# Kernel tuning notes

Hardware: AMD Instinct MI355X
Metric: run time of the kernel (lower is better)

Reference implementation:

```python
import jax, jax.numpy as jnp
import numpy as np
from jax import lax

DIM = 256
PROJ = 128
NPOS = 8          # ceil(log2(2*64+5))
EXT = 64          # attnExtension
NLAYERS = 4
HEADS = 4
KDIM = PROJ + NPOS
EPS = 1e-5


def _ln(x):
    # LayerNorm over last dim, no affine (elementwise_affine=False)
    mu = jnp.mean(x, axis=-1, keepdims=True)
    var = jnp.mean(jnp.square(x - mu), axis=-1, keepdims=True)
    return (x - mu) * lax.rsqrt(var + EPS)


def setup_inputs() -> dict:
    key = jax.random.key(0)
    ks = jax.random.split(key, 18)
    L = 2048
    s = 0.05
    return {
        "input": jax.random.normal(ks[0], (L, PROJ), jnp.float32),
        "residual": jax.random.normal(ks[1], (5 * L, DIM), jnp.float32),
        "W_proj": jax.random.normal(ks[2], (5 * DIM, KDIM), jnp.float32) * s,
        "b_proj": jnp.zeros((5 * DIM,), jnp.float32),
        "Wq": jax.random.normal(ks[3], (DIM, DIM), jnp.float32) * s,
        "bq": jnp.zeros((DIM,), jnp.float32),
        "Wk": jax.random.normal(ks[4], (DIM, KDIM), jnp.float32) * s,
        "bk": jnp.zeros((DIM,), jnp.float32),
        "Wv": jax.random.normal(ks[5], (DIM, KDIM), jnp.float32) * s,
        "bv": jnp.zeros((DIM,), jnp.float32),
        "Wo": jax.random.normal(ks[6], (DIM, DIM), jnp.float32) * s,
        "bo": jnp.zeros((DIM,), jnp.float32),
        "conv_w": jax.random.normal(ks[7], (NLAYERS, DIM, DIM, 3), jnp.float32) * s,
        "conv_b": jnp.zeros((NLAYERS, DIM), jnp.float32),
        "W_skip": jax.random.normal(ks[8], (DIM, DIM), jnp.float32) * s,
        "b_skip": jnp.zeros((DIM,), jnp.float32),
    }


def reference(input, residual, W_proj, b_proj, Wq, bq, Wk, bk, Wv, bv,
              Wo, bo, conv_w, conv_b, W_skip, b_skip):
    L = input.shape[0]
    T = 5 * L  # tgt length
    hd = DIM // HEADS

    # positional embeddings: pos[:, i] = (arange(L) % 2^(i+1)) / 2^i
    n = jnp.arange(L, dtype=input.dtype)[:, None]
    i = jnp.arange(NPOS, dtype=input.dtype)[None, :]
    pos = jnp.mod(n, 2.0 ** (i + 1.0)) / (2.0 ** i)

    src = jnp.concatenate([input, pos], axis=1)            # (L, KDIM)
    tgt = (src @ W_proj.T + b_proj).reshape(T, DIM)        # (5L, DIM)

    # banded mask: row j may attend col i iff 5i-EXT <= j < 5i+5+EXT
    j = jnp.arange(T)[:, None]
    ii = jnp.arange(L)[None, :]
    d = j - 5 * ii
    allowed = (d >= -EXT) & (d < 5 + EXT)                  # (5L, L)

    # multihead attention (eval mode, dropout skipped)
    q = (tgt @ Wq.T + bq).reshape(T, HEADS, hd).transpose(1, 0, 2)
    k = (src @ Wk.T + bk).reshape(L, HEADS, hd).transpose(1, 0, 2)
    v = (src @ Wv.T + bv).reshape(L, HEADS, hd).transpose(1, 0, 2)
    scores = jnp.einsum('hqd,hkd->hqk', q, k) / jnp.sqrt(jnp.asarray(hd, q.dtype))
    scores = jnp.where(allowed[None], scores, -jnp.inf)
    attn = jax.nn.softmax(scores, axis=-1)
    ctx = jnp.einsum('hqk,hkd->hqd', attn, v).transpose(1, 0, 2).reshape(T, DIM)
    attn_out = ctx @ Wo.T + bo

    cnn_in = _ln(attn_out) + residual                      # (5L, DIM)

    # spectral-norm conv stack (weights assumed pre-normalized) + tanh
    x = cnn_in.T[None]                                     # (1, DIM, 5L)
    for l in range(NLAYERS):
        x = jnp.tanh(
            lax.conv_general_dilated(x, conv_w[l], window_strides=(1,),
                                     padding=[(1, 1)])
            + conv_b[l][None, :, None])
    cnn_out = x[0].T                                       # (5L, DIM)

    return _ln(cnn_out + cnn_in @ W_skip.T + b_skip)
```

## Files before the change

### kernel.cpp

```cpp
#include <hip/hip_runtime.h>
#include <hip/hip_bf16.h>

#define PROJ 128
#define KPAD 192
#define EPS 1e-5f

typedef __attribute__((ext_vector_type(4))) float f32x4;
typedef __attribute__((ext_vector_type(8))) short bf16x8;
typedef __attribute__((ext_vector_type(4))) unsigned int u32x4;

__device__ inline float bflo(unsigned u){ union{unsigned x;float f;}c; c.x = u<<16; return c.f; }
__device__ inline float bfhi(unsigned u){ union{unsigned x;float f;}c; c.x = u & 0xffff0000u; return c.f; }
__device__ inline float bf2f(unsigned short u){ union{unsigned x;float f;}c; c.x = ((unsigned)u)<<16; return c.f; }
__device__ inline unsigned short f2bf(float f){
    union{float f; unsigned u;} c; c.f = f;
    unsigned r = c.u + 0x7fff + ((c.u >> 16) & 1);
    return (unsigned short)(r >> 16);
}
__device__ __forceinline__ bf16x8 asbf(u32x4 u){ union{u32x4 a; bf16x8 b;} c; c.a = u; return c.b; }

__global__ __launch_bounds__(256) void prep_all(
    const float* __restrict__ W_proj, const float* __restrict__ Wq,
    const float* __restrict__ Wk, const float* __restrict__ Wv,
    const float* __restrict__ Wo, const float* __restrict__ Ws,
    const float* __restrict__ convw, const float* __restrict__ input,
    const float* __restrict__ bq, const float* __restrict__ b_proj,
    unsigned short* __restrict__ Wqb, unsigned short* __restrict__ Wkb,
    unsigned short* __restrict__ Wvb, unsigned short* __restrict__ Wob,
    unsigned short* __restrict__ Wsb, unsigned short* __restrict__ Wcb,
    unsigned short* __restrict__ WpbT, unsigned short* __restrict__ srcb,
    unsigned short* __restrict__ cinp, float* __restrict__ zbias,
    float* __restrict__ bqc, int L, int T)
{
    int idx = blockIdx.x * 256 + threadIdx.x;
    if (idx < 81920) {
        int w = idx >> 6, lanei = idx & 63;
        int r = w >> 8, o = w & 255;
        const float* wrow = Wq + (size_t)o * 256;
        const float* bp = b_proj + r * 256;
        float s = 0.f;
        #pragma unroll
        for (int c = 0; c < 256; c += 64) s += wrow[c + lanei] * bp[c + lanei];
        #pragma unroll
        for (int m = 32; m > 0; m >>= 1) s += __shfl_xor(s, m, 64);
        if (lanei == 0) bqc[w] = s + bq[o];
        return;
    }
    idx -= 81920;
    if (idx < 65536) { Wqb[idx] = f2bf(Wq[idx]); return; }
    idx -= 65536;
    if (idx < 49152) {
        int r = idx / 192, c = idx % 192;
        Wkb[idx] = (c < 136) ? f2bf(Wk[(size_t)r * 136 + c]) : (unsigned short)0;
        return;
    }
    idx -= 49152;
    if (idx < 49152) {
        int r = idx / 192, c = idx % 192;
        Wvb[idx] = (c < 136) ? f2bf(Wv[(size_t)r * 136 + c]) : (unsigned short)0;
        return;
    }
    idx -= 49152;
    if (idx < 65536) { Wob[idx] = f2bf(Wo[idx]); return; }
    idx -= 65536;
    if (idx < 65536) {
        int e = idx & 7;
        int lane = (idx >> 3) & 63;
        int fr = (idx >> 9) & 3;
        int wid = (idx >> 11) & 7;
        int kt = idx >> 14;
        int j = fr >> 1, ks = fr & 1;
        int kq = lane >> 4, rowf = lane & 15;
        int o = wid * 32 + j * 16 + rowf;
        int c = kt * 64 + ks * 32 + kq * 8 + e;
        Wsb[idx] = f2bf(Ws[(size_t)o * 256 + c]);
        return;
    }
    idx -= 65536;
    if (idx < 786432) {
        int e = idx & 7;
        int lane = (idx >> 3) & 63;
        int fr = (idx >> 9) & 3;
        int wid = (idx >> 11) & 7;
        int ktl = idx >> 14;
        int l = ktl / 12, kt = ktl % 12;
        int j = fr >> 1, ks = fr & 1;
        int kq = lane >> 4, rowf = lane & 15;
        int o = wid * 32 + j * 16 + rowf;
        int c = kt * 64 + ks * 32 + kq * 8 + e;
        int ktap = c >> 8, ci = c & 255;
        Wcb[idx] = f2bf(convw[(((size_t)l * 256 + o) * 256 + ci) * 3 + ktap]);
        return;
    }
    idx -= 786432;
    if (idx < 327680) {
        int r = idx >> 16;
        int rem = idx & 65535;
        int c = rem >> 8, d = rem & 255;
        WpbT[idx] = (c < 136) ? f2bf(W_proj[(size_t)(r * 256 + d) * 136 + c])
                              : (unsigned short)0;
        return;
    }
    idx -= 327680;
    if (idx < L * KPAD) {
        int n = idx / KPAD, c = idx % KPAD;
        float v = 0.f;
        if (c < PROJ) v = input[(size_t)n * PROJ + c];
        else if (c < PROJ + 8) {
            int i = c - PROJ;
            int mask = (2 << i) - 1;
            v = (float)(n & mask) / (float)(1 << i);
        }
        srcb[idx] = f2bf(v);
        return;
    }
    idx -= L * KPAD;
    if (idx < 512) {
        int row = idx >> 8, c = idx & 255;
        size_t o = (row == 0) ? (size_t)c : (size_t)(T + 1) * 256 + c;
        cinp[o] = 0;
        return;
    }
    idx -= 512;
    if (idx < 256) { zbias[idx] = 0.f; return; }
}

__device__ __forceinline__ void gemm_core_64x128(
    unsigned short (&As)[64][72], unsigned short (&Bs)[128][72],
    const unsigned short* __restrict__ A, int lda,
    const unsigned short* __restrict__ B, int ldb,
    const float* __restrict__ bias,
    unsigned short* __restrict__ C, int ldc,
    int K, int m0, int n0)
{
    const int tid = threadIdx.x;
    const int lane = tid & 63;
    const int wid = tid >> 6;
    const int wm = wid >> 1, wn = wid & 1;

    const int ar = tid >> 2, asg = tid & 3;
    const int br = tid >> 1, bsg = tid & 1;

    const unsigned short* Ap = A + (size_t)(m0 + ar) * lda + asg * 16;
    const unsigned short* Bp = B + (size_t)(n0 + br) * ldb + bsg * 32;

    u32x4 ra0, ra1, rb0, rb1, rb2, rb3;
    auto loadregs = [&](int k0) {
        ra0 = *(const u32x4*)(Ap + k0);
        ra1 = *(const u32x4*)(Ap + k0 + 8);
        rb0 = *(const u32x4*)(Bp + k0);
        rb1 = *(const u32x4*)(Bp + k0 + 8);
        rb2 = *(const u32x4*)(Bp + k0 + 16);
        rb3 = *(const u32x4*)(Bp + k0 + 24);
    };
    auto stlds = [&]() {
        *(u32x4*)&As[ar][asg * 16]      = ra0;
        *(u32x4*)&As[ar][asg * 16 + 8]  = ra1;
        *(u32x4*)&Bs[br][bsg * 32]      = rb0;
        *(u32x4*)&Bs[br][bsg * 32 + 8]  = rb1;
        *(u32x4*)&Bs[br][bsg * 32 + 16] = rb2;
        *(u32x4*)&Bs[br][bsg * 32 + 24] = rb3;
    };

    f32x4 acc[2][4];
    #pragma unroll
    for (int i = 0; i < 2; ++i)
        #pragma unroll
        for (int j = 0; j < 4; ++j) acc[i][j] = (f32x4){0.f, 0.f, 0.f, 0.f};

    loadregs(0);
    stlds();
    __syncthreads();

    const int rowf = lane & 15, kb = lane >> 4;
    const int ktiles = K >> 6;
    for (int kt = 0; kt < ktiles; ++kt) {
        if (kt + 1 < ktiles) loadregs((kt + 1) << 6);
        #pragma unroll
        for (int ks = 0; ks < 2; ++ks) {
            bf16x8 af[2], bfr[4];
            #pragma unroll
            for (int i = 0; i < 2; ++i)
                af[i] = *(const bf16x8*)&As[wm * 32 + i * 16 + rowf][ks * 32 + kb * 8];
            #pragma unroll
            for (int j = 0; j < 4; ++j)
                bfr[j] = *(const bf16x8*)&Bs[wn * 64 + j * 16 + rowf][ks * 32 + kb * 8];
            #pragma unroll
            for (int i = 0; i < 2; ++i)
                #pragma unroll
                for (int j = 0; j < 4; ++j)
                    acc[i][j] = __builtin_amdgcn_mfma_f32_16x16x32_bf16(af[i], bfr[j], acc[i][j], 0, 0, 0);
        }
        __syncthreads();
        if (kt + 1 < ktiles) { stlds(); __syncthreads(); }
    }

    const int rq = lane >> 4;
    #pragma unroll
    for (int i = 0; i < 2; ++i) {
        int gm = m0 + wm * 32 + i * 16 + rq * 4;
        #pragma unroll
        for (int j = 0; j < 4; ++j) {
            int gn = n0 + wn * 64 + j * 16 + rowf;
            float bv = bias[gn];
            #pragma unroll
            for (int r = 0; r < 4; ++r)
                C[(size_t)(gm + r) * ldc + gn] = f2bf(acc[i][j][r] + bv);
        }
    }
}

__global__ __launch_bounds__(256) void combine_wq(
    const unsigned short* __restrict__ Wqb,
    const unsigned short* __restrict__ WpbT,
    const float* __restrict__ zbias,
    unsigned short* __restrict__ Wqpb)
{
    __shared__ unsigned short As[64][72];
    __shared__ unsigned short Bs[128][72];
    int bi = blockIdx.x;
    int r = bi >> 3, rem = bi & 7;
    int m0 = (rem >> 1) * 64, n0 = (rem & 1) * 128;
    gemm_core_64x128(As, Bs, Wqb, 256, WpbT + (size_t)r * 65536, 256, zbias,
                     Wqpb + (size_t)r * 65536, 256, 256, m0, n0);
}

__global__ __launch_bounds__(256) void qkv_fused(
    const unsigned short* __restrict__ srcb,
    const unsigned short* __restrict__ Wqpb,
    const unsigned short* __restrict__ Wkb,
    const unsigned short* __restrict__ Wvb,
    const float* __restrict__ bqc, const float* __restrict__ bk,
    const float* __restrict__ bv,
    unsigned short* __restrict__ qb, unsigned short* __restrict__ kb,
    unsigned short* __restrict__ vb)
{
    __shared__ unsigned short As[64][72];
    __shared__ unsigned short Bs[128][72];
    int bi = blockIdx.x;
    const unsigned short *B;
    const float* bias;
    unsigned short* C;
    int ldb, K, m0, n0, ldc;
    if (bi < 320) {
        B = Wqpb; bias = bqc; C = qb; ldb = 256; K = 192; ldc = 1280;
        m0 = (bi / 10) * 64; n0 = (bi % 10) * 128;
    } else if (bi < 384) {
        int t = bi - 320;
        B = Wkb; bias = bk; C = kb; ldb = 192; K = 192; ldc = 256;
        m0 = (t >> 1) * 64; n0 = (t & 1) * 128;
    } else {
        int t = bi - 384;
        B = Wvb; bias = bv; C = vb; ldb = 192; K = 192; ldc = 256;
        m0 = (t >> 1) * 64; n0 = (t & 1) * 128;
    }
    gemm_core_64x128(As, Bs, srcb, KPAD, B, ldb, bias, C, ldc, K, m0, n0);
}

__global__ __launch_bounds__(512) void gemm_ln0(
    const unsigned short* __restrict__ A, int lda,
    const unsigned short* __restrict__ B,
    const float* __restrict__ bias,
    const float* __restrict__ residual,
    unsigned short* __restrict__ out_bf)
{
    __shared__ unsigned short As[64][72];
    __shared__ unsigned short Bs[256][72];
    __shared__ float redS[64][4];
    __shared__ float redQ[64][4];

    const int tid = threadIdx.x;
    const int lane = tid & 63;
    const int wid = tid >> 6;
    const int wm = wid >> 2, wn = wid & 3;
    const int m0 = blockIdx.x * 64;

    const int arow = tid >> 3, acol = (tid & 7) * 8;
    const int brow = tid >> 1, bcol = (tid & 1) * 32;
    const unsigned short* Ap = A + (size_t)(m0 + arow) * lda + acol;
    const unsigned short* Bp = B + (size_t)brow * 256 + bcol;

    u32x4 ra, rb0, rb1, rb2, rb3;
    auto loadregs = [&](int k0) {
        ra  = *(const u32x4*)(Ap + k0);
        rb0 = *(const u32x4*)(Bp + k0);
        rb1 = *(const u32x4*)(Bp + k0 + 8);
        rb2 = *(const u32x4*)(Bp + k0 + 16);
        rb3 = *(const u32x4*)(Bp + k0 + 24);
    };
    auto stlds = [&]() {
        *(u32x4*)&As[arow][acol]       = ra;
        *(u32x4*)&Bs[brow][bcol]       = rb0;
        *(u32x4*)&Bs[brow][bcol + 8]   = rb1;
        *(u32x4*)&Bs[brow][bcol + 16]  = rb2;
        *(u32x4*)&Bs[brow][bcol + 24]  = rb3;
    };

    f32x4 acc[2][4];
    #pragma unroll
    for (int i = 0; i < 2; ++i)
        #pragma unroll
        for (int j = 0; j < 4; ++j) acc[i][j] = (f32x4){0.f, 0.f, 0.f, 0.f};

    loadregs(0);
    stlds();
    __syncthreads();

    const int rowf = lane & 15, kb = lane >> 4;
    #pragma unroll
    for (int kt = 0; kt < 4; ++kt) {
        if (kt < 3) loadregs((kt + 1) << 6);
        #pragma unroll
        for (int ks = 0; ks < 2; ++ks) {
            bf16x8 af[2], bfr[4];
            #pragma unroll
            for (int i = 0; i < 2; ++i)
                af[i] = *(const bf16x8*)&As[wm * 32 + i * 16 + rowf][ks * 32 + kb * 8];
            #pragma unroll
            for (int j = 0; j < 4; ++j)
                bfr[j] = *(const bf16x8*)&Bs[wn * 64 + j * 16 + rowf][ks * 32 + kb * 8];
            #pragma unroll
            for (int i = 0; i < 2; ++i)
                #pragma unroll
                for (int j = 0; j < 4; ++j)
                    acc[i][j] = __builtin_amdgcn_mfma_f32_16x16x32_bf16(af[i], bfr[j], acc[i][j], 0, 0, 0);
        }
        __syncthreads();
        if (kt < 3) { stlds(); __syncthreads(); }
    }

    const int rq = lane >> 4;
    float val[2][4][4];
    #pragma unroll
    for (int i = 0; i < 2; ++i)
        #pragma unroll
        for (int j = 0; j < 4; ++j) {
            int gn = wn * 64 + j * 16 + rowf;
            float bv = bias[gn];
            #pragma unroll
            for (int r = 0; r < 4; ++r) val[i][j][r] = acc[i][j][r] + bv;
        }

    #pragma unroll
    for (int i = 0; i < 2; ++i)
        #pragma unroll
        for (int r = 0; r < 4; ++r) {
            float s = val[i][0][r] + val[i][1][r] + val[i][2][r] + val[i][3][r];
            float q = val[i][0][r] * val[i][0][r] + val[i][1][r] * val[i][1][r]
                    + val[i][2][r] * val[i][2][r] + val[i][3][r] * val[i][3][r];
            #pragma unroll
            for (int m = 1; m < 16; m <<= 1) {
                s += __shfl_xor(s, m, 64);
                q += __shfl_xor(q, m, 64);
            }
            if (rowf == 0) {
                int row = wm * 32 + i * 16 + rq * 4 + r;
                redS[row][wn] = s;
                redQ[row][wn] = q;
            }
        }
    __syncthreads();

    #pragma unroll
    for (int i = 0; i < 2; ++i) {
        #pragma unroll
        for (int r = 0; r < 4; ++r) {
            int row = wm * 32 + i * 16 + rq * 4 + r;
            int gm = m0 + row;
            float s = redS[row][0] + redS[row][1] + redS[row][2] + redS[row][3];
            float q = redQ[row][0] + redQ[row][1] + redQ[row][2] + redQ[row][3];
            float mu = s * (1.f / 256.f);
            float var = q * (1.f / 256.f) - mu * mu;
            float rs = rsqrtf(var + EPS);
            #pragma unroll
            for (int j = 0; j < 4; ++j) {
                int gn = wn * 64 + j * 16 + rowf;
                float nv = (val[i][j][r] - mu) * rs + residual[(size_t)gm * 256 + gn];
                out_bf[(size_t)(gm + 1) * 256 + gn] = f2bf(nv);
            }
        }
    }
}

__global__ __launch_bounds__(256) void attn16(
    const unsigned short* __restrict__ q,
    const unsigned short* __restrict__ k,
    const unsigned short* __restrict__ v,
    unsigned short* __restrict__ ctx, int L)
{
    __shared__ unsigned short ksm[30][264];
    __shared__ unsigned short vsm[30][264];
    const int j0 = blockIdx.x * 16;
    const int iblk0 = (j0 >= 68) ? (j0 - 64) / 5 : 0;
    int ihim = (j0 + 79) / 5; if (ihim > L - 1) ihim = L - 1;
    const int NR = ihim - iblk0 + 1;

    for (int e = threadIdx.x; e < 30 * 32; e += 256) {
        int rr = e >> 5, cc = (e & 31) * 8;
        u32x4 kz = {0, 0, 0, 0}, vz = {0, 0, 0, 0};
        if (rr < NR) {
            kz = *(const u32x4*)&k[(size_t)(iblk0 + rr) * 256 + cc];
            vz = *(const u32x4*)&v[(size_t)(iblk0 + rr) * 256 + cc];
        }
        *(u32x4*)&ksm[rr][cc] = kz;
        *(u32x4*)&vsm[rr][cc] = vz;
    }
    __syncthreads();

    const int tid = threadIdx.x;
    const int h = tid >> 6, lane = tid & 63;
    const int qq = lane & 15, p = lane >> 4;
    const int j = j0 + qq;
    const int colb = h * 64 + p * 16;

    float qr[16];
    {
        u32x4 q0 = *(const u32x4*)&q[(size_t)j * 256 + colb];
        u32x4 q1 = *(const u32x4*)&q[(size_t)j * 256 + colb + 8];
        #pragma unroll
        for (int w = 0; w < 4; ++w) {
            qr[2 * w]     = bflo(q0[w]) * 0.125f;
            qr[2 * w + 1] = bfhi(q0[w]) * 0.125f;
            qr[8 + 2 * w]     = bflo(q1[w]) * 0.125f;
            qr[8 + 2 * w + 1] = bfhi(q1[w]) * 0.125f;
        }
    }
    const int ilo = (j >= 68) ? (j - 64) / 5 : 0;
    int ihi = (j + 64) / 5; if (ihi > L - 1) ihi = L - 1;

    float sc[30];
    #pragma unroll
    for (int t = 0; t < 30; ++t) {
        int i = iblk0 + t;
        u32x4 k0 = *(const u32x4*)&ksm[t][colb];
        u32x4 k1 = *(const u32x4*)&ksm[t][colb + 8];
        float s = 0.f;
        #pragma unroll
        for (int w = 0; w < 4; ++w) {
            s += qr[2 * w]     * bflo(k0[w]);
            s += qr[2 * w + 1] * bfhi(k0[w]);
            s += qr[8 + 2 * w]     * bflo(k1[w]);
            s += qr[8 + 2 * w + 1] * bfhi(k1[w]);
        }
        s += __shfl_xor(s, 16, 64);
        s += __shfl_xor(s, 32, 64);
        sc[t] = (i >= ilo && i <= ihi) ? s : -1e30f;
    }
    float mx = -1e30f;
    #pragma unroll
    for (int t = 0; t < 30; ++t) mx = fmaxf(mx, sc[t]);
    float den = 0.f, o[16];
    #pragma unroll
    for (int d = 0; d < 16; ++d) o[d] = 0.f;
    #pragma unroll
    for (int t = 0; t < 30; ++t) {
        float pt = __expf(sc[t] - mx);
        den += pt;
        u32x4 v0 = *(const u32x4*)&vsm[t][colb];
        u32x4 v1 = *(const u32x4*)&vsm[t][colb + 8];
        #pragma unroll
        for (int w = 0; w < 4; ++w) {
            o[2 * w]     += pt * bflo(v0[w]);
            o[2 * w + 1] += pt * bfhi(v0[w]);
            o[8 + 2 * w]     += pt * bflo(v1[w]);
            o[8 + 2 * w + 1] += pt * bfhi(v1[w]);
        }
    }
    float inv = 1.f / den;
    #pragma unroll
    for (int d = 0; d < 16; ++d)
        ctx[(size_t)j * 256 + colb + d] = f2bf(o[d] * inv);
}

#define CVALID 40

__device__ __forceinline__ void wload4a(u32x4 (&b)[4], const unsigned short* p) {
    asm volatile(
        "global_load_dwordx4 %0, %4, off\n\t"
        "global_load_dwordx4 %1, %4, off offset:1024\n\t"
        "global_load_dwordx4 %2, %4, off offset:2048\n\t"
        "global_load_dwordx4 %3, %4, off offset:3072"
        : "=&v"(b[0]), "=&v"(b[1]), "=&v"(b[2]), "=&v"(b[3])
        : "v"(p));
}
__device__ __forceinline__ void wwait8a(u32x4 (&b)[4]) {
    asm volatile("s_waitcnt vmcnt(8)" : "+v"(b[0]), "+v"(b[1]), "+v"(b[2]), "+v"(b[3]));
}
__device__ __forceinline__ void wwait4a(u32x4 (&b)[4]) {
    asm volatile("s_waitcnt vmcnt(4)" : "+v"(b[0]), "+v"(b[1]), "+v"(b[2]), "+v"(b[3]));
}
__device__ __forceinline__ void wwait0a(u32x4 (&b)[4]) {
    asm volatile("s_waitcnt vmcnt(0)" : "+v"(b[0]), "+v"(b[1]), "+v"(b[2]), "+v"(b[3]));
}

template<int NKT, bool ISCONV>
__device__ __forceinline__ void frag_gemm(
    const unsigned short* __restrict__ Wp,
    unsigned short (*actin)[264],
    f32x4 (&acc)[3][2], int wid, int lane)
{
    const int rowf = lane & 15, kq = lane >> 4;
    const unsigned short* base = Wp + wid * 2048 + lane * 8;
    u32x4 W[3][4];

    wload4a(W[0], base);
    if (NKT > 1) wload4a(W[1], base + 16384);
    if (NKT > 2) wload4a(W[2], base + 2 * 16384);
    if (NKT > 2)      wwait8a(W[0]);
    else if (NKT > 1) wwait4a(W[0]);
    else              wwait0a(W[0]);

    #pragma unroll
    for (int kt = 0; kt < NKT; ++kt) {
        u32x4 (&cur)[4] = W[kt % 3];
        const int dt = ISCONV ? (kt >> 2) : 1;
        const int cb = ISCONV ? ((kt & 3) * 64) : (kt * 64);
        #pragma unroll
        for (int ks = 0; ks < 2; ++ks) {
            bf16x8 a0 = *(const bf16x8*)&actin[rowf + dt][cb + ks * 32 + kq * 8];
            bf16x8 a1 = *(const bf16x8*)&actin[16 + rowf + dt][cb + ks * 32 + kq * 8];
            bf16x8 a2 = *(const bf16x8*)&actin[32 + rowf + dt][cb + ks * 32 + kq * 8];
            bf16x8 w0 = asbf(ks ? cur[1] : cur[0]);
            bf16x8 w1 = asbf(ks ? cur[3] : cur[2]);
            acc[0][0] = __builtin_amdgcn_mfma_f32_16x16x32_bf16(a0, w0, acc[0][0], 0, 0, 0);
            acc[0][1] = __builtin_amdgcn_mfma_f32_16x16x32_bf16(a0, w1, acc[0][1], 0, 0, 0);
            acc[1][0] = __builtin_amdgcn_mfma_f32_16x16x32_bf16(a1, w0, acc[1][0], 0, 0, 0);
            acc[1][1] = __builtin_amdgcn_mfma_f32_16x16x32_bf16(a1, w1, acc[1][1], 0, 0, 0);
            acc[2][0] = __builtin_amdgcn_mfma_f32_16x16x32_bf16(a2, w0, acc[2][0], 0, 0, 0);
            acc[2][1] = __builtin_amdgcn_mfma_f32_16x16x32_bf16(a2, w1, acc[2][1], 0, 0, 0);
        }
        if (kt + 3 < NKT) {
            wload4a(cur, base + (size_t)(kt + 3) * 16384);
            wwait8a(W[(kt + 1) % 3]);
        } else if (kt + 2 < NKT) {
            wwait4a(W[(kt + 1) % 3]);
        } else if (kt + 1 < NKT) {
            wwait0a(W[(kt + 1) % 3]);
        }
    }
}

__global__ __launch_bounds__(512)
__attribute__((amdgpu_waves_per_eu(2)))
void conv_skip_ln(
    const unsigned short* __restrict__ cinp,
    const unsigned short* __restrict__ Wcb,
    const float* __restrict__ conv_b,
    const unsigned short* __restrict__ Wsb,
    const float* __restrict__ b_skip,
    float* __restrict__ out, int T)
{
    __shared__ unsigned short actA[50][264];
    __shared__ unsigned short actB[50][264];
    __shared__ float redS[48][8];
    __shared__ float redQ[48][8];

    const int tid = threadIdx.x;
    const int lane = tid & 63;
    const int wid = tid >> 6;
    const int rowf = lane & 15;
    const int kq = lane >> 4;
    const int t0 = blockIdx.x * CVALID;

    for (int e = tid; e < 50 * 32; e += 512) {
        int b = e >> 5, c = (e & 31) * 8;
        int g = t0 - 5 + b;
        u32x4 z = {0, 0, 0, 0};
        if (g >= -1 && g <= T)
            z = *(const u32x4*)&cinp[(size_t)(g + 1) * 256 + c];
        *(u32x4*)&actA[b][c] = z;
    }
    if (tid < 256) actB[0][tid] = 0; else actB[49][tid - 256] = 0;
    __syncthreads();

    f32x4 skipacc[3][2];
    #pragma unroll
    for (int i = 0; i < 3; ++i)
        #pragma unroll
        for (int j = 0; j < 2; ++j) skipacc[i][j] = (f32x4){0.f, 0.f, 0.f, 0.f};
    frag_gemm<4, false>(Wsb, actA, skipacc, wid, lane);

    const int gn0 = wid * 32 + rowf;
    f32x4 cacc[3][2];
    #pragma unroll 1
    for (int l = 0; l < 4; ++l) {
        #pragma unroll
        for (int i = 0; i < 3; ++i)
            #pragma unroll
            for (int j = 0; j < 2; ++j) cacc[i][j] = (f32x4){0.f, 0.f, 0.f, 0.f};
        unsigned short (*ain)[264]  = (l & 1) ? actB : actA;
        unsigned short (*aout)[264] = (l & 1) ? actA : actB;
        frag_gemm<12, true>(Wcb + (size_t)l * 196608, ain, cacc, wid, lane);

        float b0 = conv_b[l * 256 + gn0];
        float b1 = conv_b[l * 256 + gn0 + 16];
        if (l < 3) {
            #pragma unroll
            for (int i = 0; i < 3; ++i)
                #pragma unroll
                for (int r = 0; r < 4; ++r) {
                    int w = i * 16 + kq * 4 + r;
                    int g = t0 - 4 + w;
                    bool ok = (g >= 0 && g < T);
                    float v0 = cacc[i][0][r] + b0;
                    float v1 = cacc[i][1][r] + b1;
                    v0 = 1.f - 2.f / (__expf(2.f * v0) + 1.f);
                    v1 = 1.f - 2.f / (__expf(2.f * v1) + 1.f);
                    aout[w + 1][gn0]      = ok ? f2bf(v0) : (unsigned short)0;
                    aout[w + 1][gn0 + 16] = ok ? f2bf(v1) : (unsigned short)0;
                }
            if (tid < 256) aout[0][tid] = 0; else aout[49][tid - 256] = 0;
            __syncthreads();
        } else {
            float sb0 = b_skip[gn0], sb1 = b_skip[gn0 + 16];
            #pragma unroll
            for (int i = 0; i < 3; ++i)
                #pragma unroll
                for (int r = 0; r < 4; ++r) {
                    int w = i * 16 + kq * 4 + r;
                    int g = t0 - 4 + w;
                    bool ok = (g >= 0 && g < T);
                    float v0 = cacc[i][0][r] + b0;
                    float v1 = cacc[i][1][r] + b1;
                    v0 = ok ? (1.f - 2.f / (__expf(2.f * v0) + 1.f)) : 0.f;
                    v1 = ok ? (1.f - 2.f / (__expf(2.f * v1) + 1.f)) : 0.f;
                    skipacc[i][0][r] += sb0 + v0;
                    skipacc[i][1][r] += sb1 + v1;
                }
        }
    }

    #pragma unroll
    for (int i = 0; i < 3; ++i)
        #pragma unroll
        for (int r = 0; r < 4; ++r) {
            float a = skipacc[i][0][r], b = skipacc[i][1][r];
            float s = a + b;
            float q = a * a + b * b;
            #pragma unroll
            for (int m = 1; m < 16; m <<= 1) {
                s += __shfl_xor(s, m, 64);
                q += __shfl_xor(q, m, 64);
            }
            if (rowf == 0) {
                int row = i * 16 + kq * 4 + r;
                redS[row][wid] = s;
                redQ[row][wid] = q;
            }
        }
    __syncthreads();

    #pragma unroll
    for (int i = 0; i < 3; ++i)
        #pragma unroll
        for (int r = 0; r < 4; ++r) {
            int row = i * 16 + kq * 4 + r;
            if (row < 4 || row >= 44) continue;
            int g = t0 - 4 + row;
            if (g >= T) continue;
            float s = 0.f, q = 0.f;
            #pragma unroll
            for (int x = 0; x < 8; ++x) { s += redS[row][x]; q += redQ[row][x]; }
            float mu = s * (1.f / 256.f);
            float var = q * (1.f / 256.f) - mu * mu;
            float rs = rsqrtf(var + EPS);
            out[(size_t)g * 256 + gn0]      = (skipacc[i][0][r] - mu) * rs;
            out[(size_t)g * 256 + gn0 + 16] = (skipacc[i][1][r] - mu) * rs;
        }
}

extern "C" void kernel_launch(void* const* d_in, const int* in_sizes, int n_in,
                              void* d_out, int out_size, void* d_ws, size_t ws_size,
                              hipStream_t stream) {
    const float* input    = (const float*)d_in[0];
    const float* residual = (const float*)d_in[1];
    const float* W_proj   = (const float*)d_in[2];
    const float* b_proj   = (const float*)d_in[3];
    const float* Wq       = (const float*)d_in[4];
    const float* bq       = (const float*)d_in[5];
    const float* Wk       = (const float*)d_in[6];
    const float* bk       = (const float*)d_in[7];
    const float* Wv       = (const float*)d_in[8];
    const float* bv       = (const float*)d_in[9];
    const float* Wo       = (const float*)d_in[10];
    const float* bo       = (const float*)d_in[11];
    const float* conv_w   = (const float*)d_in[12];
    const float* conv_b   = (const float*)d_in[13];
    const float* W_skip   = (const float*)d_in[14];
    const float* b_skip   = (const float*)d_in[15];
    float* out = (float*)d_out;

    const int L = in_sizes[0] / PROJ;
    const int T = 5 * L;

    unsigned short* w16 = (unsigned short*)d_ws;
    size_t off = 0;
    auto alloc = [&](size_t n) { unsigned short* p = w16 + off; off += n; return p; };
    unsigned short* Wqb   = alloc(65536);
    unsigned short* Wkb   = alloc(49152);
    unsigned short* Wvb   = alloc(49152);
    unsigned short* Wob   = alloc(65536);
    unsigned short* Wsb   = alloc(65536);
    unsigned short* Wcb   = alloc(786432);
    unsigned short* WpbT  = alloc(327680);
    unsigned short* Wqpb  = alloc(327680);
    unsigned short* srcb  = alloc((size_t)L * KPAD);
    unsigned short* tgtb  = alloc((size_t)T * 256);
    unsigned short* qb    = alloc((size_t)T * 256);
    unsigned short* kb    = alloc((size_t)L * 256);
    unsigned short* vb    = alloc((size_t)L * 256);
    unsigned short* cinp  = alloc((size_t)(T + 2) * 256);
    float* zbias = (float*)alloc(512);
    float* bqc   = (float*)alloc(2560);

    prep_all<<<dim3(7363), 256, 0, stream>>>(
        W_proj, Wq, Wk, Wv, Wo, W_skip, conv_w, input, bq, b_proj,
        Wqb, Wkb, Wvb, Wob, Wsb, Wcb, WpbT, srcb, cinp, zbias, bqc, L, T);

    combine_wq<<<dim3(40), 256, 0, stream>>>(Wqb, WpbT, zbias, Wqpb);

    qkv_fused<<<dim3(448), 256, 0, stream>>>(
        srcb, Wqpb, Wkb, Wvb, bqc, bk, bv, qb, kb, vb);

    attn16<<<dim3(T / 16), 256, 0, stream>>>(qb, kb, vb, tgtb, L);

    gemm_ln0<<<dim3(T / 64), 512, 0, stream>>>(tgtb, 256, Wob, bo, residual, cinp);

    conv_skip_ln<<<dim3(T / CVALID), 512, 0, stream>>>(
        cinp, Wcb, conv_b, Wsb, b_skip, out, T);
}
```

Baseline: 88.59 us.

## Fuse out-projection and LayerNorm into conv kernel, vectorize weight prep

Measured after the change: 85.16 us. -3.9%, faster.

```diff
diff --git a/kernel.cpp b/kernel.cpp
--- a/kernel.cpp
+++ b/kernel.cpp
@@ -4,6 +4,7 @@
 #define PROJ 128
 #define KPAD 192
 #define EPS 1e-5f
+#define CVALID 40
 
 typedef __attribute__((ext_vector_type(4))) float f32x4;
 typedef __attribute__((ext_vector_type(8))) short bf16x8;
@@ -18,6 +19,9 @@
     return (unsigned short)(r >> 16);
 }
 __device__ __forceinline__ bf16x8 asbf(u32x4 u){ union{u32x4 a; bf16x8 b;} c; c.a = u; return c.b; }
+__device__ __forceinline__ unsigned pk2(float a, float b){
+    return (unsigned)f2bf(a) | ((unsigned)f2bf(b) << 16);
+}
 
 __global__ __launch_bounds__(256) void prep_all(
     const float* __restrict__ W_proj, const float* __restrict__ Wq,
@@ -29,8 +33,7 @@
     unsigned short* __restrict__ Wvb, unsigned short* __restrict__ Wob,
     unsigned short* __restrict__ Wsb, unsigned short* __restrict__ Wcb,
     unsigned short* __restrict__ WpbT, unsigned short* __restrict__ srcb,
-    unsigned short* __restrict__ cinp, float* __restrict__ zbias,
-    float* __restrict__ bqc, int L, int T)
+    float* __restrict__ zbias, float* __restrict__ bqc, int L)
 {
     int idx = blockIdx.x * 256 + threadIdx.x;
     if (idx < 81920) {
@@ -47,81 +50,91 @@
         return;
     }
     idx -= 81920;
-    if (idx < 65536) { Wqb[idx] = f2bf(Wq[idx]); return; }
-    idx -= 65536;
-    if (idx < 49152) {
-        int r = idx / 192, c = idx % 192;
-        Wkb[idx] = (c < 136) ? f2bf(Wk[(size_t)r * 136 + c]) : (unsigned short)0;
+    if (idx < 8192) {
+        const float* s = Wq + (size_t)idx * 8;
+        *(u32x4*)&Wqb[(size_t)idx * 8] =
+            (u32x4){pk2(s[0],s[1]), pk2(s[2],s[3]), pk2(s[4],s[5]), pk2(s[6],s[7])};
         return;
     }
-    idx -= 49152;
-    if (idx < 49152) {
-        int r = idx / 192, c = idx % 192;
-        Wvb[idx] = (c < 136) ? f2bf(Wv[(size_t)r * 136 + c]) : (unsigned short)0;
+    idx -= 8192;
+    if (idx < 12288) {
+        int which = idx / 6144, t = idx % 6144;
+        int r = t / 24, c0 = (t % 24) * 8;
+        const float* W = which ? Wv : Wk;
+        unsigned short* D = which ? Wvb : Wkb;
+        u32x4 v = {0,0,0,0};
+        if (c0 < 136) {
+            const float* s = W + (size_t)r * 136 + c0;
+            v = (u32x4){pk2(s[0],s[1]), pk2(s[2],s[3]), pk2(s[4],s[5]), pk2(s[6],s[7])};
+        }
+        *(u32x4*)&D[(size_t)r * 192 + c0] = v;
         return;
     }
-    idx -= 49152;
-    if (idx < 65536) { Wob[idx] = f2bf(Wo[idx]); return; }
-    idx -= 65536;
-    if (idx < 65536) {
-        int e = idx & 7;
-        int lane = (idx >> 3) & 63;
-        int fr = (idx >> 9) & 3;
-        int wid = (idx >> 11) & 7;
-        int kt = idx >> 14;
-        int j = fr >> 1, ks = fr & 1;
-        int kq = lane >> 4, rowf = lane & 15;
-        int o = wid * 32 + j * 16 + rowf;
-        int c = kt * 64 + ks * 32 + kq * 8 + e;
-        Wsb[idx] = f2bf(Ws[(size_t)o * 256 + c]);
+    idx -= 12288;
+    if (idx < 16384) {
+        int which = idx / 8192, t = idx % 8192;
+        int lane = t & 63, fr = (t >> 6) & 3, wid = (t >> 8) & 7, kt = t >> 11;
+        int o = wid * 32 + (fr >> 1) * 16 + (lane & 15);
+        int c = kt * 64 + (fr & 1) * 32 + (lane >> 4) * 8;
+        const float* s = (which ? Ws : Wo) + (size_t)o * 256 + c;
+        unsigned short* D = which ? Wsb : Wob;
+        *(u32x4*)&D[(size_t)t * 8] =
+            (u32x4){pk2(s[0],s[1]), pk2(s[2],s[3]), pk2(s[4],s[5]), pk2(s[6],s[7])};
         return;
     }
-    idx -= 65536;
-    if (idx < 786432) {
-        int e = idx & 7;
-        int lane = (idx >> 3) & 63;
-        int fr = (idx >> 9) & 3;
-        int wid = (idx >> 11) & 7;
-        int ktl = idx >> 14;
+    idx -= 16384;
+    if (idx < 98304) {
+        int t = idx;
+        int lane = t & 63, fr = (t >> 6) & 3, wid = (t >> 8) & 7, ktl = t >> 11;
         int l = ktl / 12, kt = ktl % 12;
-        int j = fr >> 1, ks = fr & 1;
-        int kq = lane >> 4, rowf = lane & 15;
-        int o = wid * 32 + j * 16 + rowf;
-        int c = kt * 64 + ks * 32 + kq * 8 + e;
+        int o = wid * 32 + (fr >> 1) * 16 + (lane & 15);
+        int c = kt * 64 + (fr & 1) * 32 + (lane >> 4) * 8;
         int ktap = c >> 8, ci = c & 255;
-        Wcb[idx] = f2bf(convw[(((size_t)l * 256 + o) * 256 + ci) * 3 + ktap]);
+        const float* s = convw + (((size_t)l * 256 + o) * 256 + ci) * 3 + ktap;
+        float v[8];
+        #pragma unroll
+        for (int j = 0; j < 8; ++j) v[j] = s[(size_t)j * 3];
+        *(u32x4*)&Wcb[(size_t)t * 8] =
+            (u32x4){pk2(v[0],v[1]), pk2(v[2],v[3]), pk2(v[4],v[5]), pk2(v[6],v[7])};
         return;
     }
-    idx -= 786432;
-    if (idx < 327680) {
-        int r = idx >> 16;
-        int rem = idx & 65535;
-        int c = rem >> 8, d = rem & 255;
-        WpbT[idx] = (c < 136) ? f2bf(W_proj[(size_t)(r * 256 + d) * 136 + c])
-                              : (unsigned short)0;
+    idx -= 98304;
+    if (idx < 40960) {
+        int t = idx;
+        int r = t >> 13;
+        int c = (t >> 5) & 255;
+        int d0 = (t & 31) * 8;
+        u32x4 v = {0,0,0,0};
+        if (c < 136) {
+            const float* s = W_proj + ((size_t)(r * 256 + d0)) * 136 + c;
+            float x[8];
+            #pragma unroll
+            for (int j = 0; j < 8; ++j) x[j] = s[(size_t)j * 136];
+            v = (u32x4){pk2(x[0],x[1]), pk2(x[2],x[3]), pk2(x[4],x[5]), pk2(x[6],x[7])};
+        }
+        *(u32x4*)&WpbT[(size_t)t * 8] = v;
         return;
     }
-    idx -= 327680;
-    if (idx < L * KPAD) {
-        int n = idx / KPAD, c = idx % KPAD;
-        float v = 0.f;
-        if (c < PROJ) v = input[(size_t)n * PROJ + c];
-        else if (c < PROJ + 8) {
-            int i = c - PROJ;
-            int mask = (2 << i) - 1;
-            v = (float)(n & mask) / (float)(1 << i);
-        }
-        srcb[idx] = f2bf(v);
+    idx -= 40960;
+    if (idx < L * 24) {
+        int n = idx / 24, c0 = (idx % 24) * 8;
+        u32x4 v = {0,0,0,0};
+        if (c0 < PROJ) {
+            const float* s = input + (size_t)n * PROJ + c0;
+            v = (u32x4){pk2(s[0],s[1]), pk2(s[2],s[3]), pk2(s[4],s[5]), pk2(s[6],s[7])};
+        } else if (c0 == PROJ) {
+            float p[8];
+            #pragma unroll
+            for (int i = 0; i < 8; ++i) {
+                int mask = (2 << i) - 1;
+                p[i] = (float)(n & mask) / (float)(1 << i);
+            }
+            v = (u32x4){pk2(p[0],p[1]), pk2(p[2],p[3]), pk2(p[4],p[5]), pk2(p[6],p[7])};
+        }
+        *(u32x4*)&srcb[(size_t)n * KPAD + c0] = v;
         return;
     }
-    idx -= L * KPAD;
-    if (idx < 512) {
-        int row = idx >> 8, c = idx & 255;
-        size_t o = (row == 0) ? (size_t)c : (size_t)(T + 1) * 256 + c;
-        cinp[o] = 0;
-        return;
-    }
-    idx -= 512;
+    idx -= L * 24;
     if (idx < 256) { zbias[idx] = 0.f; return; }
 }
 
@@ -257,131 +270,6 @@
     gemm_core_64x128(As, Bs, srcb, KPAD, B, ldb, bias, C, ldc, K, m0, n0);
 }
 
-__global__ __launch_bounds__(512) void gemm_ln0(
-    const unsigned short* __restrict__ A, int lda,
-    const unsigned short* __restrict__ B,
-    const float* __restrict__ bias,
-    const float* __restrict__ residual,
-    unsigned short* __restrict__ out_bf)
-{
-    __shared__ unsigned short As[64][72];
-    __shared__ unsigned short Bs[256][72];
-    __shared__ float redS[64][4];
-    __shared__ float redQ[64][4];
-
-    const int tid = threadIdx.x;
-    const int lane = tid & 63;
-    const int wid = tid >> 6;
-    const int wm = wid >> 2, wn = wid & 3;
-    const int m0 = blockIdx.x * 64;
-
-    const int arow = tid >> 3, acol = (tid & 7) * 8;
-    const int brow = tid >> 1, bcol = (tid & 1) * 32;
-    const unsigned short* Ap = A + (size_t)(m0 + arow) * lda + acol;
-    const unsigned short* Bp = B + (size_t)brow * 256 + bcol;
-
-    u32x4 ra, rb0, rb1, rb2, rb3;
-    auto loadregs = [&](int k0) {
-        ra  = *(const u32x4*)(Ap + k0);
-        rb0 = *(const u32x4*)(Bp + k0);
-        rb1 = *(const u32x4*)(Bp + k0 + 8);
-        rb2 = *(const u32x4*)(Bp + k0 + 16);
-        rb3 = *(const u32x4*)(Bp + k0 + 24);
-    };
-    auto stlds = [&]() {
-        *(u32x4*)&As[arow][acol]       = ra;
-        *(u32x4*)&Bs[brow][bcol]       = rb0;
-        *(u32x4*)&Bs[brow][bcol + 8]   = rb1;
-        *(u32x4*)&Bs[brow][bcol + 16]  = rb2;
-        *(u32x4*)&Bs[brow][bcol + 24]  = rb3;
-    };
-
-    f32x4 acc[2][4];
-    #pragma unroll
-    for (int i = 0; i < 2; ++i)
-        #pragma unroll
-        for (int j = 0; j < 4; ++j) acc[i][j] = (f32x4){0.f, 0.f, 0.f, 0.f};
-
-    loadregs(0);
-    stlds();
-    __syncthreads();
-
-    const int rowf = lane & 15, kb = lane >> 4;
-    #pragma unroll
-    for (int kt = 0; kt < 4; ++kt) {
-        if (kt < 3) loadregs((kt + 1) << 6);
-        #pragma unroll
-        for (int ks = 0; ks < 2; ++ks) {
-            bf16x8 af[2], bfr[4];
-            #pragma unroll
-            for (int i = 0; i < 2; ++i)
-                af[i] = *(const bf16x8*)&As[wm * 32 + i * 16 + rowf][ks * 32 + kb * 8];
-            #pragma unroll
-            for (int j = 0; j < 4; ++j)
-                bfr[j] = *(const bf16x8*)&Bs[wn * 64 + j * 16 + rowf][ks * 32 + kb * 8];
-            #pragma unroll
-            for (int i = 0; i < 2; ++i)
-                #pragma unroll
-                for (int j = 0; j < 4; ++j)
-                    acc[i][j] = __builtin_amdgcn_mfma_f32_16x16x32_bf16(af[i], bfr[j], acc[i][j], 0, 0, 0);
-        }
-        __syncthreads();
-        if (kt < 3) { stlds(); __syncthreads(); }
-    }
-
-    const int rq = lane >> 4;
-    float val[2][4][4];
-    #pragma unroll
-    for (int i = 0; i < 2; ++i)
-        #pragma unroll
-        for (int j = 0; j < 4; ++j) {
-            int gn = wn * 64 + j * 16 + rowf;
-            float bv = bias[gn];
-            #pragma unroll
-            for (int r = 0; r < 4; ++r) val[i][j][r] = acc[i][j][r] + bv;
-        }
-
-    #pragma unroll
-    for (int i = 0; i < 2; ++i)
-        #pragma unroll
-        for (int r = 0; r < 4; ++r) {
-            float s = val[i][0][r] + val[i][1][r] + val[i][2][r] + val[i][3][r];
-            float q = val[i][0][r] * val[i][0][r] + val[i][1][r] * val[i][1][r]
-                    + val[i][2][r] * val[i][2][r] + val[i][3][r] * val[i][3][r];
-            #pragma unroll
-            for (int m = 1; m < 16; m <<= 1) {
-                s += __shfl_xor(s, m, 64);
-                q += __shfl_xor(q, m, 64);
-            }
-            if (rowf == 0) {
-                int row = wm * 32 + i * 16 + rq * 4 + r;
-                redS[row][wn] = s;
-                redQ[row][wn] = q;
-            }
-        }
-    __syncthreads();
-
-    #pragma unroll
-    for (int i = 0; i < 2; ++i) {
-        #pragma unroll
-        for (int r = 0; r < 4; ++r) {
-            int row = wm * 32 + i * 16 + rq * 4 + r;
-            int gm = m0 + row;
-            float s = redS[row][0] + redS[row][1] + redS[row][2] + redS[row][3];
-            float q = redQ[row][0] + redQ[row][1] + redQ[row][2] + redQ[row][3];
-            float mu = s * (1.f / 256.f);
-            float var = q * (1.f / 256.f) - mu * mu;
-            float rs = rsqrtf(var + EPS);
-            #pragma unroll
-            for (int j = 0; j < 4; ++j) {
-                int gn = wn * 64 + j * 16 + rowf;
-                float nv = (val[i][j][r] - mu) * rs + residual[(size_t)gm * 256 + gn];
-                out_bf[(size_t)(gm + 1) * 256 + gn] = f2bf(nv);
-            }
-        }
-    }
-}
-
 __global__ __launch_bounds__(256) void attn16(
     const unsigned short* __restrict__ q,
     const unsigned short* __restrict__ k,
@@ -472,8 +360,6 @@
         ctx[(size_t)j * 256 + colb + d] = f2bf(o[d] * inv);
 }
 
-#define CVALID 40
-
 __device__ __forceinline__ void wload4a(u32x4 (&b)[4], const unsigned short* p) {
     asm volatile(
         "global_load_dwordx4 %0, %4, off\n\t"
@@ -493,11 +379,11 @@
     asm volatile("s_waitcnt vmcnt(0)" : "+v"(b[0]), "+v"(b[1]), "+v"(b[2]), "+v"(b[3]));
 }
 
-template<int NKT, bool ISCONV>
+template<int NKT, int DTMODE, int NROW>
 __device__ __forceinline__ void frag_gemm(
     const unsigned short* __restrict__ Wp,
-    unsigned short (*actin)[264],
-    f32x4 (&acc)[3][2], int wid, int lane)
+    const unsigned short (*actin)[264],
+    f32x4 (&acc)[NROW][2], int wid, int lane)
 {
     const int rowf = lane & 15, kq = lane >> 4;
     const unsigned short* base = Wp + wid * 2048 + lane * 8;
@@ -513,21 +399,18 @@
     #pragma unroll
     for (int kt = 0; kt < NKT; ++kt) {
         u32x4 (&cur)[4] = W[kt % 3];
-        const int dt = ISCONV ? (kt >> 2) : 1;
-        const int cb = ISCONV ? ((kt & 3) * 64) : (kt * 64);
+        const int dt = (DTMODE == 0) ? (kt >> 2) : (DTMODE == 1 ? 1 : 0);
+        const int cb = (DTMODE == 0) ? ((kt & 3) * 64) : (kt * 64);
         #pragma unroll
         for (int ks = 0; ks < 2; ++ks) {
-            bf16x8 a0 = *(const bf16x8*)&actin[rowf + dt][cb + ks * 32 + kq * 8];
-            bf16x8 a1 = *(const bf16x8*)&actin[16 + rowf + dt][cb + ks * 32 + kq * 8];
-            bf16x8 a2 = *(const bf16x8*)&actin[32 + rowf + dt][cb + ks * 32 + kq * 8];
             bf16x8 w0 = asbf(ks ? cur[1] : cur[0]);
             bf16x8 w1 = asbf(ks ? cur[3] : cur[2]);
-            acc[0][0] = __builtin_amdgcn_mfma_f32_16x16x32_bf16(a0, w0, acc[0][0], 0, 0, 0);
-            acc[0][1] = __builtin_amdgcn_mfma_f32_16x16x32_bf16(a0, w1, acc[0][1], 0, 0, 0);
-            acc[1][0] = __builtin_amdgcn_mfma_f32_16x16x32_bf16(a1, w0, acc[1][0], 0, 0, 0);
-            acc[1][1] = __builtin_amdgcn_mfma_f32_16x16x32_bf16(a1, w1, acc[1][1], 0, 0, 0);
-            acc[2][0] = __builtin_amdgcn_mfma_f32_16x16x32_bf16(a2, w0, acc[2][0], 0, 0, 0);
-            acc[2][1] = __builtin_amdgcn_mfma_f32_16x16x32_bf16(a2, w1, acc[2][1], 0, 0, 0);
+            #pragma unroll
+            for (int i = 0; i < NROW; ++i) {
+                bf16x8 a = *(const bf16x8*)&actin[i * 16 + rowf + dt][cb + ks * 32 + kq * 8];
+                acc[i][0] = __builtin_amdgcn_mfma_f32_16x16x32_bf16(a, w0, acc[i][0], 0, 0, 0);
+                acc[i][1] = __builtin_amdgcn_mfma_f32_16x16x32_bf16(a, w1, acc[i][1], 0, 0, 0);
+            }
         }
         if (kt + 3 < NKT) {
             wload4a(cur, base + (size_t)(kt + 3) * 16384);
@@ -542,8 +425,11 @@
 
 __global__ __launch_bounds__(512)
 __attribute__((amdgpu_waves_per_eu(2)))
-void conv_skip_ln(
-    const unsigned short* __restrict__ cinp,
+void conv_mega(
+    const unsigned short* __restrict__ ctx,
+    const float* __restrict__ residual,
+    const unsigned short* __restrict__ Wob,
+    const float* __restrict__ bo,
     const unsigned short* __restrict__ Wcb,
     const float* __restrict__ conv_b,
     const unsigned short* __restrict__ Wsb,
@@ -551,9 +437,9 @@
     float* __restrict__ out, int T)
 {
     __shared__ unsigned short actA[50][264];
-    __shared__ unsigned short actB[50][264];
-    __shared__ float redS[48][8];
-    __shared__ float redQ[48][8];
+    __shared__ unsigned short actB[64][264];
+    __shared__ float redS[64][8];
+    __shared__ float redQ[64][8];
 
     const int tid = threadIdx.x;
     const int lane = tid & 63;
@@ -561,40 +447,90 @@
     const int rowf = lane & 15;
     const int kq = lane >> 4;
     const int t0 = blockIdx.x * CVALID;
-
-    for (int e = tid; e < 50 * 32; e += 512) {
+    const int gn0 = wid * 32 + rowf;
+
+    for (int e = tid; e < 64 * 32; e += 512) {
         int b = e >> 5, c = (e & 31) * 8;
         int g = t0 - 5 + b;
         u32x4 z = {0, 0, 0, 0};
-        if (g >= -1 && g <= T)
-            z = *(const u32x4*)&cinp[(size_t)(g + 1) * 256 + c];
-        *(u32x4*)&actA[b][c] = z;
-    }
-    if (tid < 256) actB[0][tid] = 0; else actB[49][tid - 256] = 0;
+        if (g >= 0 && g < T)
+            z = *(const u32x4*)&ctx[(size_t)g * 256 + c];
+        *(u32x4*)&actB[b][c] = z;
+    }
     __syncthreads();
 
+    f32x4 wacc[4][2];
+    #pragma unroll
+    for (int i = 0; i < 4; ++i)
+        #pragma unroll
+        for (int j = 0; j < 2; ++j) wacc[i][j] = (f32x4){0.f, 0.f, 0.f, 0.f};
+    frag_gemm<4, 2, 4>(Wob, actB, wacc, wid, lane);
+
+    float bo0 = bo[gn0], bo1 = bo[gn0 + 16];
+    #pragma unroll
+    for (int i = 0; i < 4; ++i)
+        #pragma unroll
+        for (int r = 0; r < 4; ++r) {
+            float a = wacc[i][0][r] + bo0;
+            float b = wacc[i][1][r] + bo1;
+            wacc[i][0][r] = a; wacc[i][1][r] = b;
+            float s = a + b;
+            float q = a * a + b * b;
+            #pragma unroll
+            for (int m = 1; m < 16; m <<= 1) {
+                s += __shfl_xor(s, m, 64);
+                q += __shfl_xor(q, m, 64);
+            }
+            if (rowf == 0) {
+                int row = i * 16 + kq * 4 + r;
+                redS[row][wid] = s;
+                redQ[row][wid] = q;
+            }
+        }
+    __syncthreads();
+
+    #pragma unroll
+    for (int i = 0; i < 4; ++i)
+        #pragma unroll
+        for (int r = 0; r < 4; ++r) {
+            int row = i * 16 + kq * 4 + r;
+            if (row >= 50) continue;
+            int g = t0 - 5 + row;
+            float s = 0.f, q = 0.f;
+            #pragma unroll
+            for (int x = 0; x < 8; ++x) { s += redS[row][x]; q += redQ[row][x]; }
+            float mu = s * (1.f / 256.f);
+            float var = q * (1.f / 256.f) - mu * mu;
+            float rs = rsqrtf(var + EPS);
+            unsigned short o0 = 0, o1 = 0;
+            if (g >= 0 && g < T) {
+                o0 = f2bf((wacc[i][0][r] - mu) * rs + residual[(size_t)g * 256 + gn0]);
+                o1 = f2bf((wacc[i][1][r] - mu) * rs + residual[(size_t)g * 256 + gn0 + 16]);
+            }
+            actA[row][gn0]      = o0;
+            actA[row][gn0 + 16] = o1;
+        }
+    __syncthreads();
+
     f32x4 skipacc[3][2];
     #pragma unroll
     for (int i = 0; i < 3; ++i)
         #pragma unroll
         for (int j = 0; j < 2; ++j) skipacc[i][j] = (f32x4){0.f, 0.f, 0.f, 0.f};
-    frag_gemm<4, false>(Wsb, actA, skipacc, wid, lane);
-
-    const int gn0 = wid * 32 + rowf;
+    frag_gemm<4, 1, 3>(Wsb, actA, skipacc, wid, lane);
+
     f32x4 cacc[3][2];
     #pragma unroll 1
-    for (int l = 0; l < 4; ++l) {
+    for (int l2 = 0; l2 < 2; ++l2) {
+        const int le = 2 * l2;
         #pragma unroll
         for (int i = 0; i < 3; ++i)
             #pragma unroll
             for (int j = 0; j < 2; ++j) cacc[i][j] = (f32x4){0.f, 0.f, 0.f, 0.f};
-        unsigned short (*ain)[264]  = (l & 1) ? actB : actA;
-        unsigned short (*aout)[264] = (l & 1) ? actA : actB;
-        frag_gemm<12, true>(Wcb + (size_t)l * 196608, ain, cacc, wid, lane);
-
-        float b0 = conv_b[l * 256 + gn0];
-        float b1 = conv_b[l * 256 + gn0 + 16];
-        if (l < 3) {
+        frag_gemm<12, 0, 3>(Wcb + (size_t)le * 196608, actA, cacc, wid, lane);
+        {
+            float b0 = conv_b[le * 256 + gn0];
+            float b1 = conv_b[le * 256 + gn0 + 16];
             #pragma unroll
             for (int i = 0; i < 3; ++i)
                 #pragma unroll
@@ -606,27 +542,56 @@
                     float v1 = cacc[i][1][r] + b1;
                     v0 = 1.f - 2.f / (__expf(2.f * v0) + 1.f);
                     v1 = 1.f - 2.f / (__expf(2.f * v1) + 1.f);
-                    aout[w + 1][gn0]      = ok ? f2bf(v0) : (unsigned short)0;
-                    aout[w + 1][gn0 + 16] = ok ? f2bf(v1) : (unsigned short)0;
+                    actB[w + 1][gn0]      = ok ? f2bf(v0) : (unsigned short)0;
+                    actB[w + 1][gn0 + 16] = ok ? f2bf(v1) : (unsigned short)0;
                 }
-            if (tid < 256) aout[0][tid] = 0; else aout[49][tid - 256] = 0;
+            if (tid < 256) actB[0][tid] = 0; else actB[49][tid - 256] = 0;
             __syncthreads();
-        } else {
-            float sb0 = b_skip[gn0], sb1 = b_skip[gn0 + 16];
-            #pragma unroll
-            for (int i = 0; i < 3; ++i)
+        }
+
+        const int lo = 2 * l2 + 1;
+        #pragma unroll
+        for (int i = 0; i < 3; ++i)
+            #pragma unroll
+            for (int j = 0; j < 2; ++j) cacc[i][j] = (f32x4){0.f, 0.f, 0.f, 0.f};
+        frag_gemm<12, 0, 3>(Wcb + (size_t)lo * 196608, actB, cacc, wid, lane);
+        {
+            float b0 = conv_b[lo * 256 + gn0];
+            float b1 = conv_b[lo * 256 + gn0 + 16];
+            if (l2 == 0) {
                 #pragma unroll
-                for (int r = 0; r < 4; ++r) {
-                    int w = i * 16 + kq * 4 + r;
-                    int g = t0 - 4 + w;
-                    bool ok = (g >= 0 && g < T);
-                    float v0 = cacc[i][0][r] + b0;
-                    float v1 = cacc[i][1][r] + b1;
-                    v0 = ok ? (1.f - 2.f / (__expf(2.f * v0) + 1.f)) : 0.f;
-                    v1 = ok ? (1.f - 2.f / (__expf(2.f * v1) + 1.f)) : 0.f;
-                    skipacc[i][0][r] += sb0 + v0;
-                    skipacc[i][1][r] += sb1 + v1;
-                }
+                for (int i = 0; i < 3; ++i)
+                    #pragma unroll
+                    for (int r = 0; r < 4; ++r) {
+                        int w = i * 16 + kq * 4 + r;
+                        int g = t0 - 4 + w;
+                        bool ok = (g >= 0 && g < T);
+                        float v0 = cacc[i][0][r] + b0;
+                        float v1 = cacc[i][1][r] + b1;
+                        v0 = 1.f - 2.f / (__expf(2.f * v0) + 1.f);
+                        v1 = 1.f - 2.f / (__expf(2.f * v1) + 1.f);
+                        actA[w + 1][gn0]      = ok ? f2bf(v0) : (unsigned short)0;
+                        actA[w + 1][gn0 + 16] = ok ? f2bf(v1) : (unsigned short)0;
+                    }
+                if (tid < 256) actA[0][tid] = 0; else actA[49][tid - 256] = 0;
+                __syncthreads();
+            } else {
+                float sb0 = b_skip[gn0], sb1 = b_skip[gn0 + 16];
+                #pragma unroll
+                for (int i = 0; i < 3; ++i)
+                    #pragma unroll
+                    for (int r = 0; r < 4; ++r) {
+                        int w = i * 16 + kq * 4 + r;
+                        int g = t0 - 4 + w;
+                        bool ok = (g >= 0 && g < T);
+                        float v0 = cacc[i][0][r] + b0;
+                        float v1 = cacc[i][1][r] + b1;
+                        v0 = ok ? (1.f - 2.f / (__expf(2.f * v0) + 1.f)) : 0.f;
+                        v1 = ok ? (1.f - 2.f / (__expf(2.f * v1) + 1.f)) : 0.f;
+                        skipacc[i][0][r] += sb0 + v0;
+                        skipacc[i][1][r] += sb1 + v1;
+                    }
+            }
         }
     }
 
@@ -709,13 +674,12 @@
     unsigned short* qb    = alloc((size_t)T * 256);
     unsigned short* kb    = alloc((size_t)L * 256);
     unsigned short* vb    = alloc((size_t)L * 256);
-    unsigned short* cinp  = alloc((size_t)(T + 2) * 256);
     float* zbias = (float*)alloc(512);
     float* bqc   = (float*)alloc(2560);
 
-    prep_all<<<dim3(7363), 256, 0, stream>>>(
+    prep_all<<<dim3(1201), 256, 0, stream>>>(
         W_proj, Wq, Wk, Wv, Wo, W_skip, conv_w, input, bq, b_proj,
-        Wqb, Wkb, Wvb, Wob, Wsb, Wcb, WpbT, srcb, cinp, zbias, bqc, L, T);
+        Wqb, Wkb, Wvb, Wob, Wsb, Wcb, WpbT, srcb, zbias, bqc, L);
 
     combine_wq<<<dim3(40), 256, 0, stream>>>(Wqb, WpbT, zbias, Wqpb);
 
@@ -724,8 +688,6 @@
 
     attn16<<<dim3(T / 16), 256, 0, stream>>>(qb, kb, vb, tgtb, L);
 
-    gemm_ln0<<<dim3(T / 64), 512, 0, stream>>>(tgtb, 256, Wob, bo, residual, cinp);
-
-    conv_skip_ln<<<dim3(T / CVALID), 512, 0, stream>>>(
-        cinp, Wcb, conv_b, Wsb, b_skip, out, T);
-}
+    conv_mega<<<dim3(T / CVALID), 512, 0, stream>>>(
+        tgtb, residual, Wob, bo, Wcb, conv_b, Wsb, b_skip, out, T);
+}
```
